# Performance work log

Hardware: AMD Instinct MI355X
Metric: run time of the kernel (lower is better)

The kernel has to match this reference:

```python
import jax, jax.numpy as jnp
import numpy as np

N = 100000          # total nodes
F = 128             # in_features
B = 1000            # number of graphs
NPG = 100           # nodes per graph (contiguous)
DEG = 16            # avg degree
E = B * NPG * DEG   # total edges (intra-graph)
K_RATIO = 0.8
KNUM = max(1, int(K_RATIO * NPG))  # nodes kept per graph = 80


def setup_inputs() -> dict:
    key = jax.random.key(0)
    k1, k2, k3, k4 = jax.random.split(key, 4)
    x = jax.random.normal(k1, (N, F), dtype=jnp.float32)
    # intra-graph random edges: offset each block of NPG*DEG edges by its graph's base node id
    offs = (jnp.arange(E, dtype=jnp.int32) // (NPG * DEG)) * NPG
    src = jax.random.randint(k2, (E,), 0, NPG, dtype=jnp.int32) + offs
    dst = jax.random.randint(k3, (E,), 0, NPG, dtype=jnp.int32) + offs
    edge_index = jnp.stack([src, dst], axis=0)
    batch = (jnp.arange(N, dtype=jnp.int32) // NPG).astype(jnp.int32)
    limit = float(np.sqrt(6.0 / (F + 1)))  # xavier_uniform for (F,1)
    theta_att = jax.random.uniform(k4, (F, 1), dtype=jnp.float32, minval=-limit, maxval=limit)
    return {"x": x, "edge_index": edge_index, "batch": batch, "theta_att": theta_att}


def reference(x, edge_index, batch, theta_att):
    num_nodes = x.shape[0]
    # add self loops with weight 1
    loops = jnp.arange(num_nodes, dtype=edge_index.dtype)
    row = jnp.concatenate([edge_index[0], loops])
    col = jnp.concatenate([edge_index[1], loops])
    w = jnp.ones(row.shape[0], dtype=x.dtype)
    # symmetric degree normalization (degree counted over row, as in torch code)
    deg = jax.ops.segment_sum(w, row, num_segments=num_nodes)
    dis = jnp.where(deg > 0, jax.lax.rsqrt(deg), jnp.zeros((), x.dtype))
    norm = dis[row] * w * dis[col]
    # scatter-add: agg[dst] += x[src] * norm
    agg = jax.ops.segment_sum(x[row] * norm[:, None], col, num_segments=num_nodes)
    z = (agg @ theta_att)[:, 0]                     # (N,)
    # per-graph top-k: graphs are contiguous and equal-sized -> reshape
    zb = z.reshape(B, NPG)
    _, pos = jax.lax.top_k(zb, KNUM)                # (B, KNUM) positions within each graph
    pos = jnp.sort(pos, axis=1)                     # global sort of keep_idx == per-graph sort here
    keep = (pos + jnp.arange(B, dtype=pos.dtype)[:, None] * NPG).reshape(-1)  # (B*KNUM,)
    scale = jax.nn.sigmoid(z[keep])[:, None]
    x_new = x[keep] * scale                         # (B*KNUM, F)
    batch_new = batch[keep]
    # subgraph with relabeled nodes; dropped edges padded with -1 (fixed shape for jit)
    node_mask = jnp.zeros(num_nodes, dtype=bool).at[keep].set(True)
    new_id = jnp.cumsum(node_mask.astype(jnp.int32)) - 1
    emask = node_mask[edge_index[0]] & node_mask[edge_index[1]]
    edge_index_new = jnp.where(emask[None, :], new_id[edge_index], -1)
    return x_new, edge_index_new, batch_new
```

## Files before the change

### kernel.cpp

```cpp
#include <hip/hip_runtime.h>


#define NPG   100
#define EPG   1600
#define KNUM  80
#define FDIM  128
#define BT    512
#define NF4   (NPG * FDIM / 4)
#define NE4   (EPG / 4)
#define NCH   (NF4 / BT)
#define NREM  (NF4 - NCH * BT)
#define P8    9

struct Smem {
    alignas(16) float xB[NPG * FDIM];
    int4   edge4[NE4];
    int    cnt[8][NPG];
    double part[NPG * P8];
    double dis[NPG];
    double a[NPG];
    double zp[8][NPG];
    double z[NPG];
    unsigned long long mask7[8];
    int    newid[NPG];
    float  scalen[NPG];
};

typedef __attribute__((address_space(1))) const unsigned int gu32;
typedef __attribute__((address_space(3))) unsigned int lu32;

__device__ __forceinline__ void bar_nodrain() {
    asm volatile("s_waitcnt lgkmcnt(0)" ::: "memory");
    __builtin_amdgcn_s_barrier();
    asm volatile("" ::: "memory");
}

template<bool FROMLDS, bool PF>
__device__ __forceinline__
void process_graph(Smem& sm, int g, int tid, int wave, int lane, float4 th,
                   float4 (&v)[NCH], float4& vR, int4 es, int4 ed,
                   const float4* pfsrc,
                   float* __restrict__ out, int E_total, int out_x_elems)
{
    const int  base = g * NPG;
    const bool hasE = tid < NE4;
    const bool hasR = tid < NREM;
    int* sh_edge = (int*)sm.edge4;

    {
        int*    cw = sm.cnt[wave];
        double* zw = sm.zp[wave];
        for (int i = lane; i < NPG; i += 64) { cw[i] = 0; zw[i] = 0.0; }
    }

    int4 p;
    if (hasE) {
        int4 s4 = es, d4 = ed;
        s4.x -= base; s4.y -= base; s4.z -= base; s4.w -= base;
        d4.x -= base; d4.y -= base; d4.z -= base; d4.w -= base;
        p.x = s4.x | (d4.x << 16); p.y = s4.y | (d4.y << 16);
        p.z = s4.z | (d4.z << 16); p.w = s4.w | (d4.w << 16);
        sm.edge4[tid] = p;
        int* cw = sm.cnt[wave];
        atomicAdd(&cw[s4.x], 1); atomicAdd(&cw[s4.y], 1);
        atomicAdd(&cw[s4.z], 1); atomicAdd(&cw[s4.w], 1);
    }

    const float4* xl = (const float4*)sm.xB;
    #pragma unroll
    for (int i = 0; i < NCH; ++i) {
        int idx = i * BT + tid;
        if (FROMLDS) v[i] = xl[idx];
        double dp = (double)v[i].x * th.x + (double)v[i].y * th.y
                  + (double)v[i].z * th.z + (double)v[i].w * th.w;
        dp += __shfl_xor(dp, 1, 64);
        dp += __shfl_xor(dp, 2, 64);
        if ((lane & 3) == 0)
            sm.part[(idx >> 5) * P8 + ((idx & 31) >> 2)] = dp;
    }
    if (hasR) {
        int idx = NCH * BT + tid;
        if (FROMLDS) vR = xl[idx];
        double dp = (double)vR.x * th.x + (double)vR.y * th.y
                  + (double)vR.z * th.z + (double)vR.w * th.w;
        dp += __shfl_xor(dp, 1, 64);
        dp += __shfl_xor(dp, 2, 64);
        if ((lane & 3) == 0)
            sm.part[(idx >> 5) * P8 + ((idx & 31) >> 2)] = dp;
    }

    if (PF) {
        #pragma unroll
        for (int i = 0; i < NCH; ++i) {
            int idx = i * BT + tid;
            __builtin_amdgcn_global_load_lds((gu32*)(pfsrc + idx),
                (lu32*)(sm.xB + (size_t)(i * BT + wave * 64) * 4), 16, 0, 0);
        }
        if (wave < 2) {
            int idx = NCH * BT + tid;
            __builtin_amdgcn_global_load_lds((gu32*)(pfsrc + idx),
                (lu32*)(sm.xB + (size_t)(NCH * BT + wave * 64) * 4), 16, 0, 0);
        }
    }
    bar_nodrain();

    if (tid < NPG) {
        const double* pr = sm.part + tid * P8;
        double s = ((pr[0] + pr[1]) + (pr[2] + pr[3]))
                 + ((pr[4] + pr[5]) + (pr[6] + pr[7]));
        int deg = 1 + sm.cnt[0][tid] + sm.cnt[1][tid] + sm.cnt[2][tid]
                    + sm.cnt[3][tid] + sm.cnt[4][tid] + sm.cnt[5][tid]
                    + sm.cnt[6][tid] + sm.cnt[7][tid];
        double dis = 1.0 / sqrt((double)deg);
        sm.dis[tid] = dis;
        sm.a[tid]   = s * dis;
    }
    bar_nodrain();

    {
        double* zw = sm.zp[wave];
        for (int j = tid; j < EPG; j += BT) {
            int e = sh_edge[j];
            atomicAdd(&zw[e >> 16], sm.a[e & 0xffff]);
        }
    }
    bar_nodrain();

    if (tid < NPG) {
        double zi = sm.a[tid]
                  + sm.zp[0][tid] + sm.zp[1][tid] + sm.zp[2][tid] + sm.zp[3][tid]
                  + sm.zp[4][tid] + sm.zp[5][tid] + sm.zp[6][tid] + sm.zp[7][tid];
        sm.z[tid] = zi * sm.dis[tid];
        sm.newid[tid] = -1;
    }
    bar_nodrain();

    const bool rk = tid < 4 * NPG;
    const int  n2 = tid >> 2;
    int r = 0;
    double zn = 0.0;
    if (rk) {
        zn = sm.z[n2];
        const int j0 = (tid & 3) * 25;
        for (int j = j0; j < j0 + 25; ++j) {
            double zj = sm.z[j];
            r += (int)((zj > zn) | ((zj == zn) & (j < n2)));
        }
    }
    r += __shfl_xor(r, 1, 64);
    r += __shfl_xor(r, 2, 64);
    const bool lead = rk && ((tid & 3) == 0) && (r < KNUM);
    unsigned long long m = __ballot(lead);
    if (lane == 0) sm.mask7[wave] = m;
    bar_nodrain();

    if (lead) {
        int before = __popcll(m & ((1ull << lane) - 1ull));
        for (int w2 = 0; w2 < wave; ++w2) before += __popcll(sm.mask7[w2]);
        int row = g * KNUM + before;
        sm.newid[n2]  = row;
        sm.scalen[n2] = 1.0f / (1.0f + __expf(-(float)zn));
        out[(size_t)out_x_elems + 2 * (size_t)E_total + row] = (float)g;
    }
    bar_nodrain();

    float4* outx = (float4*)out;
    #pragma unroll
    for (int i = 0; i < NCH; ++i) {
        int idx = i * BT + tid;
        int nid = sm.newid[idx >> 5];
        if (nid >= 0) {
            float sc = sm.scalen[idx >> 5];
            float4 o;
            o.x = v[i].x * sc; o.y = v[i].y * sc;
            o.z = v[i].z * sc; o.w = v[i].w * sc;
            outx[(size_t)nid * 32 + (idx & 31)] = o;
        }
    }
    if (hasR) {
        int idx = NCH * BT + tid;
        int nid = sm.newid[idx >> 5];
        if (nid >= 0) {
            float sc = sm.scalen[idx >> 5];
            float4 o;
            o.x = vR.x * sc; o.y = vR.y * sc;
            o.z = vR.z * sc; o.w = vR.w * sc;
            outx[(size_t)nid * 32 + (idx & 31)] = o;
        }
    }

    float* e0 = out + out_x_elems;
    float* e1 = e0 + E_total;
    if (hasE) {
        float4 o0, o1;
        {
            int a_ = sm.newid[p.x & 0xffff], b_ = sm.newid[p.x >> 16];
            bool vv = (a_ >= 0) && (b_ >= 0);
            o0.x = vv ? (float)a_ : -1.0f; o1.x = vv ? (float)b_ : -1.0f;
        }
        {
            int a_ = sm.newid[p.y & 0xffff], b_ = sm.newid[p.y >> 16];
            bool vv = (a_ >= 0) && (b_ >= 0);
            o0.y = vv ? (float)a_ : -1.0f; o1.y = vv ? (float)b_ : -1.0f;
        }
        {
            int a_ = sm.newid[p.z & 0xffff], b_ = sm.newid[p.z >> 16];
            bool vv = (a_ >= 0) && (b_ >= 0);
            o0.z = vv ? (float)a_ : -1.0f; o1.z = vv ? (float)b_ : -1.0f;
        }
        {
            int a_ = sm.newid[p.w & 0xffff], b_ = sm.newid[p.w >> 16];
            bool vv = (a_ >= 0) && (b_ >= 0);
            o0.w = vv ? (float)a_ : -1.0f; o1.w = vv ? (float)b_ : -1.0f;
        }
        ((float4*)e0)[(size_t)g * NE4 + tid] = o0;
        ((float4*)e1)[(size_t)g * NE4 + tid] = o1;
    }
}

__global__ __launch_bounds__(BT, 4)
void sagpool_fused8(const float* __restrict__ x,
                    const int*   __restrict__ ei,
                    const float* __restrict__ theta,
                    float* __restrict__ out,
                    int E_total, int out_x_elems, int n_graphs)
{
    __shared__ Smem sm;
    const int tid  = threadIdx.x;
    const int wave = tid >> 6;
    const int lane = tid & 63;
    const int gA   = blockIdx.x * 2;
    const int gB   = gA + 1;
    const bool hasE = tid < NE4;
    const bool hasR = tid < NREM;
    const bool doB  = gB < n_graphs;

    const float4 th = ((const float4*)theta)[lane & 31];

    int4 esA = {0,0,0,0}, edA = {0,0,0,0}, esB = {0,0,0,0}, edB = {0,0,0,0};
    if (hasE) {
        esA = ((const int4*)(ei + (size_t)gA * EPG))[tid];
        edA = ((const int4*)(ei + (size_t)E_total + (size_t)gA * EPG))[tid];
        if (doB) {
            esB = ((const int4*)(ei + (size_t)gB * EPG))[tid];
            edB = ((const int4*)(ei + (size_t)E_total + (size_t)gB * EPG))[tid];
        }
    }
    float4 v[NCH];
    float4 vR = {0.f, 0.f, 0.f, 0.f};
    const float4* xA = (const float4*)(x + (size_t)gA * NPG * FDIM);
    const float4* xB = (const float4*)(x + (size_t)gB * NPG * FDIM);
    #pragma unroll
    for (int i = 0; i < NCH; ++i) v[i] = xA[i * BT + tid];
    if (hasR) vR = xA[NCH * BT + tid];

    process_graph<false, true>(sm, gA, tid, wave, lane, th, v, vR, esA, edA,
                               xB, out, E_total, out_x_elems);
    if (doB) {
        __syncthreads();
        process_graph<true, false>(sm, gB, tid, wave, lane, th, v, vR, esB, edB,
                                   nullptr, out, E_total, out_x_elems);
    }
}

extern "C" void kernel_launch(void* const* d_in, const int* in_sizes, int n_in,
                              void* d_out, int out_size, void* d_ws, size_t ws_size,
                              hipStream_t stream)
{
    const float* x     = (const float*)d_in[0];
    const int*   ei    = (const int*)d_in[1];
    const float* theta = (const float*)d_in[3];
    float* out = (float*)d_out;

    const int N = in_sizes[0] / FDIM;
    const int E = in_sizes[1] / 2;
    const int B = N / NPG;
    const int out_x_elems = B * KNUM * FDIM;
    const int nb = (B + 1) / 2;

    sagpool_fused8<<<dim3(nb), dim3(BT), 0, stream>>>(x, ei, theta, out,
                                                      E, out_x_elems, B);
}
```

Baseline: 112.5 us.

## Overlap graph A output stores with graph B setup and dot-product phase

Restructures the two-graph-per-block kernel so graph A's scaled feature rows and relabeled edges are computed into registers first. Their global stores are then issued after graph B's edge packing and dot products, instead of before graph B starts. The intent is to hide store latency and the full __syncthreads between graphs behind graph B's work, replacing that sync with lighter barriers. In exchange it holds more live registers (nidA plus the edge payloads), which risks spills or lower occupancy under the launch bound of 4.

```diff
diff --git a/kernel.cpp b/kernel.cpp
--- a/kernel.cpp
+++ b/kernel.cpp
@@ -35,74 +35,11 @@
     asm volatile("" ::: "memory");
 }
 
-template<bool FROMLDS, bool PF>
 __device__ __forceinline__
-void process_graph(Smem& sm, int g, int tid, int wave, int lane, float4 th,
-                   float4 (&v)[NCH], float4& vR, int4 es, int4 ed,
-                   const float4* pfsrc,
-                   float* __restrict__ out, int E_total, int out_x_elems)
-{
-    const int  base = g * NPG;
-    const bool hasE = tid < NE4;
-    const bool hasR = tid < NREM;
+void mid_phases(Smem& sm, int g, int tid, int wave, int lane,
+                float* __restrict__ out, int E_total, int out_x_elems)
+{
     int* sh_edge = (int*)sm.edge4;
-
-    {
-        int*    cw = sm.cnt[wave];
-        double* zw = sm.zp[wave];
-        for (int i = lane; i < NPG; i += 64) { cw[i] = 0; zw[i] = 0.0; }
-    }
-
-    int4 p;
-    if (hasE) {
-        int4 s4 = es, d4 = ed;
-        s4.x -= base; s4.y -= base; s4.z -= base; s4.w -= base;
-        d4.x -= base; d4.y -= base; d4.z -= base; d4.w -= base;
-        p.x = s4.x | (d4.x << 16); p.y = s4.y | (d4.y << 16);
-        p.z = s4.z | (d4.z << 16); p.w = s4.w | (d4.w << 16);
-        sm.edge4[tid] = p;
-        int* cw = sm.cnt[wave];
-        atomicAdd(&cw[s4.x], 1); atomicAdd(&cw[s4.y], 1);
-        atomicAdd(&cw[s4.z], 1); atomicAdd(&cw[s4.w], 1);
-    }
-
-    const float4* xl = (const float4*)sm.xB;
-    #pragma unroll
-    for (int i = 0; i < NCH; ++i) {
-        int idx = i * BT + tid;
-        if (FROMLDS) v[i] = xl[idx];
-        double dp = (double)v[i].x * th.x + (double)v[i].y * th.y
-                  + (double)v[i].z * th.z + (double)v[i].w * th.w;
-        dp += __shfl_xor(dp, 1, 64);
-        dp += __shfl_xor(dp, 2, 64);
-        if ((lane & 3) == 0)
-            sm.part[(idx >> 5) * P8 + ((idx & 31) >> 2)] = dp;
-    }
-    if (hasR) {
-        int idx = NCH * BT + tid;
-        if (FROMLDS) vR = xl[idx];
-        double dp = (double)vR.x * th.x + (double)vR.y * th.y
-                  + (double)vR.z * th.z + (double)vR.w * th.w;
-        dp += __shfl_xor(dp, 1, 64);
-        dp += __shfl_xor(dp, 2, 64);
-        if ((lane & 3) == 0)
-            sm.part[(idx >> 5) * P8 + ((idx & 31) >> 2)] = dp;
-    }
-
-    if (PF) {
-        #pragma unroll
-        for (int i = 0; i < NCH; ++i) {
-            int idx = i * BT + tid;
-            __builtin_amdgcn_global_load_lds((gu32*)(pfsrc + idx),
-                (lu32*)(sm.xB + (size_t)(i * BT + wave * 64) * 4), 16, 0, 0);
-        }
-        if (wave < 2) {
-            int idx = NCH * BT + tid;
-            __builtin_amdgcn_global_load_lds((gu32*)(pfsrc + idx),
-                (lu32*)(sm.xB + (size_t)(NCH * BT + wave * 64) * 4), 16, 0, 0);
-        }
-    }
-    bar_nodrain();
 
     if (tid < NPG) {
         const double* pr = sm.part + tid * P8;
@@ -163,63 +100,52 @@
         out[(size_t)out_x_elems + 2 * (size_t)E_total + row] = (float)g;
     }
     bar_nodrain();
-
-    float4* outx = (float4*)out;
-    #pragma unroll
-    for (int i = 0; i < NCH; ++i) {
-        int idx = i * BT + tid;
-        int nid = sm.newid[idx >> 5];
-        if (nid >= 0) {
-            float sc = sm.scalen[idx >> 5];
-            float4 o;
-            o.x = v[i].x * sc; o.y = v[i].y * sc;
-            o.z = v[i].z * sc; o.w = v[i].w * sc;
-            outx[(size_t)nid * 32 + (idx & 31)] = o;
-        }
-    }
-    if (hasR) {
-        int idx = NCH * BT + tid;
-        int nid = sm.newid[idx >> 5];
-        if (nid >= 0) {
-            float sc = sm.scalen[idx >> 5];
-            float4 o;
-            o.x = vR.x * sc; o.y = vR.y * sc;
-            o.z = vR.z * sc; o.w = vR.w * sc;
-            outx[(size_t)nid * 32 + (idx & 31)] = o;
-        }
-    }
-
-    float* e0 = out + out_x_elems;
-    float* e1 = e0 + E_total;
-    if (hasE) {
-        float4 o0, o1;
-        {
-            int a_ = sm.newid[p.x & 0xffff], b_ = sm.newid[p.x >> 16];
-            bool vv = (a_ >= 0) && (b_ >= 0);
-            o0.x = vv ? (float)a_ : -1.0f; o1.x = vv ? (float)b_ : -1.0f;
-        }
-        {
-            int a_ = sm.newid[p.y & 0xffff], b_ = sm.newid[p.y >> 16];
-            bool vv = (a_ >= 0) && (b_ >= 0);
-            o0.y = vv ? (float)a_ : -1.0f; o1.y = vv ? (float)b_ : -1.0f;
-        }
-        {
-            int a_ = sm.newid[p.z & 0xffff], b_ = sm.newid[p.z >> 16];
-            bool vv = (a_ >= 0) && (b_ >= 0);
-            o0.z = vv ? (float)a_ : -1.0f; o1.z = vv ? (float)b_ : -1.0f;
-        }
-        {
-            int a_ = sm.newid[p.w & 0xffff], b_ = sm.newid[p.w >> 16];
-            bool vv = (a_ >= 0) && (b_ >= 0);
-            o0.w = vv ? (float)a_ : -1.0f; o1.w = vv ? (float)b_ : -1.0f;
-        }
-        ((float4*)e0)[(size_t)g * NE4 + tid] = o0;
-        ((float4*)e1)[(size_t)g * NE4 + tid] = o1;
-    }
+}
+
+__device__ __forceinline__
+int4 pack_edges(Smem& sm, int base, int tid, int wave, int4 es, int4 ed)
+{
+    int4 s4 = es, d4 = ed;
+    s4.x -= base; s4.y -= base; s4.z -= base; s4.w -= base;
+    d4.x -= base; d4.y -= base; d4.z -= base; d4.w -= base;
+    int4 p; p.x = s4.x | (d4.x << 16); p.y = s4.y | (d4.y << 16);
+            p.z = s4.z | (d4.z << 16); p.w = s4.w | (d4.w << 16);
+    sm.edge4[tid] = p;
+    int* cw = sm.cnt[wave];
+    atomicAdd(&cw[s4.x], 1); atomicAdd(&cw[s4.y], 1);
+    atomicAdd(&cw[s4.z], 1); atomicAdd(&cw[s4.w], 1);
+    return p;
+}
+
+__device__ __forceinline__
+float4 edge_payload(Smem& sm, int4 p, bool lo)
+{
+    float4 o;
+    {
+        int a_ = sm.newid[p.x & 0xffff], b_ = sm.newid[p.x >> 16];
+        bool vv = (a_ >= 0) && (b_ >= 0);
+        o.x = vv ? (float)(lo ? a_ : b_) : -1.0f;
+    }
+    {
+        int a_ = sm.newid[p.y & 0xffff], b_ = sm.newid[p.y >> 16];
+        bool vv = (a_ >= 0) && (b_ >= 0);
+        o.y = vv ? (float)(lo ? a_ : b_) : -1.0f;
+    }
+    {
+        int a_ = sm.newid[p.z & 0xffff], b_ = sm.newid[p.z >> 16];
+        bool vv = (a_ >= 0) && (b_ >= 0);
+        o.z = vv ? (float)(lo ? a_ : b_) : -1.0f;
+    }
+    {
+        int a_ = sm.newid[p.w & 0xffff], b_ = sm.newid[p.w >> 16];
+        bool vv = (a_ >= 0) && (b_ >= 0);
+        o.w = vv ? (float)(lo ? a_ : b_) : -1.0f;
+    }
+    return o;
 }
 
 __global__ __launch_bounds__(BT, 4)
-void sagpool_fused8(const float* __restrict__ x,
+void sagpool_fused9(const float* __restrict__ x,
                     const int*   __restrict__ ei,
                     const float* __restrict__ theta,
                     float* __restrict__ out,
@@ -236,6 +162,9 @@
     const bool doB  = gB < n_graphs;
 
     const float4 th = ((const float4*)theta)[lane & 31];
+    float4* outx = (float4*)out;
+    float* e0 = out + out_x_elems;
+    float* e1 = e0 + E_total;
 
     int4 esA = {0,0,0,0}, edA = {0,0,0,0}, esB = {0,0,0,0}, edB = {0,0,0,0};
     if (hasE) {
@@ -254,12 +183,172 @@
     for (int i = 0; i < NCH; ++i) v[i] = xA[i * BT + tid];
     if (hasR) vR = xA[NCH * BT + tid];
 
-    process_graph<false, true>(sm, gA, tid, wave, lane, th, v, vR, esA, edA,
-                               xB, out, E_total, out_x_elems);
+    {
+        int*    cw = sm.cnt[wave];
+        double* zw = sm.zp[wave];
+        for (int i = lane; i < NPG; i += 64) { cw[i] = 0; zw[i] = 0.0; }
+    }
+    int4 pA = {0,0,0,0};
+    if (hasE) pA = pack_edges(sm, gA * NPG, tid, wave, esA, edA);
+
+    #pragma unroll
+    for (int i = 0; i < NCH; ++i) {
+        int idx = i * BT + tid;
+        double dp = (double)v[i].x * th.x + (double)v[i].y * th.y
+                  + (double)v[i].z * th.z + (double)v[i].w * th.w;
+        dp += __shfl_xor(dp, 1, 64);
+        dp += __shfl_xor(dp, 2, 64);
+        if ((lane & 3) == 0)
+            sm.part[(idx >> 5) * P8 + ((idx & 31) >> 2)] = dp;
+    }
+    if (hasR) {
+        int idx = NCH * BT + tid;
+        double dp = (double)vR.x * th.x + (double)vR.y * th.y
+                  + (double)vR.z * th.z + (double)vR.w * th.w;
+        dp += __shfl_xor(dp, 1, 64);
+        dp += __shfl_xor(dp, 2, 64);
+        if ((lane & 3) == 0)
+            sm.part[(idx >> 5) * P8 + ((idx & 31) >> 2)] = dp;
+    }
+
     if (doB) {
-        __syncthreads();
-        process_graph<true, false>(sm, gB, tid, wave, lane, th, v, vR, esB, edB,
-                                   nullptr, out, E_total, out_x_elems);
+        #pragma unroll
+        for (int i = 0; i < NCH; ++i) {
+            int idx = i * BT + tid;
+            __builtin_amdgcn_global_load_lds((gu32*)(xB + idx),
+                (lu32*)(sm.xB + (size_t)(i * BT + wave * 64) * 4), 16, 0, 0);
+        }
+        if (wave < 2) {
+            int idx = NCH * BT + tid;
+            __builtin_amdgcn_global_load_lds((gu32*)(xB + idx),
+                (lu32*)(sm.xB + (size_t)(NCH * BT + wave * 64) * 4), 16, 0, 0);
+        }
+    }
+    bar_nodrain();
+
+    mid_phases(sm, gA, tid, wave, lane, out, E_total, out_x_elems);
+
+    int nidA[NCH], nidAR = -1;
+    #pragma unroll
+    for (int i = 0; i < NCH; ++i) {
+        int row = (i * BT + tid) >> 5;
+        int nid = sm.newid[row];
+        nidA[i] = nid;
+        if (nid >= 0) {
+            float sc = sm.scalen[row];
+            v[i].x *= sc; v[i].y *= sc; v[i].z *= sc; v[i].w *= sc;
+        }
+    }
+    if (hasR) {
+        int row = (NCH * BT + tid) >> 5;
+        nidAR = sm.newid[row];
+        if (nidAR >= 0) {
+            float sc = sm.scalen[row];
+            vR.x *= sc; vR.y *= sc; vR.z *= sc; vR.w *= sc;
+        }
+    }
+    float4 o0A = {0,0,0,0}, o1A = {0,0,0,0};
+    if (hasE) {
+        o0A = edge_payload(sm, pA, true);
+        o1A = edge_payload(sm, pA, false);
+    }
+    bar_nodrain();
+
+    if (!doB) {
+        #pragma unroll
+        for (int i = 0; i < NCH; ++i) {
+            int idx = i * BT + tid;
+            if (nidA[i] >= 0) outx[(size_t)nidA[i] * 32 + (idx & 31)] = v[i];
+        }
+        if (hasR && nidAR >= 0)
+            outx[(size_t)nidAR * 32 + ((NCH * BT + tid) & 31)] = vR;
+        if (hasE) {
+            ((float4*)e0)[(size_t)gA * NE4 + tid] = o0A;
+            ((float4*)e1)[(size_t)gA * NE4 + tid] = o1A;
+        }
+        return;
+    }
+
+    {
+        int*    cw = sm.cnt[wave];
+        double* zw = sm.zp[wave];
+        for (int i = lane; i < NPG; i += 64) { cw[i] = 0; zw[i] = 0.0; }
+    }
+    int4 pB = {0,0,0,0};
+    if (hasE) pB = pack_edges(sm, gB * NPG, tid, wave, esB, edB);
+
+    asm volatile("s_waitcnt vmcnt(0)" ::: "memory");
+
+    const float4* xl = (const float4*)sm.xB;
+    #pragma unroll
+    for (int i = 0; i < NCH; ++i) {
+        int idx = i * BT + tid;
+        float4 w4 = xl[idx];
+        double dp = (double)w4.x * th.x + (double)w4.y * th.y
+                  + (double)w4.z * th.z + (double)w4.w * th.w;
+        dp += __shfl_xor(dp, 1, 64);
+        dp += __shfl_xor(dp, 2, 64);
+        if ((lane & 3) == 0)
+            sm.part[(idx >> 5) * P8 + ((idx & 31) >> 2)] = dp;
+    }
+    if (hasR) {
+        int idx = NCH * BT + tid;
+        float4 w4 = xl[idx];
+        double dp = (double)w4.x * th.x + (double)w4.y * th.y
+                  + (double)w4.z * th.z + (double)w4.w * th.w;
+        dp += __shfl_xor(dp, 1, 64);
+        dp += __shfl_xor(dp, 2, 64);
+        if ((lane & 3) == 0)
+            sm.part[(idx >> 5) * P8 + ((idx & 31) >> 2)] = dp;
+    }
+
+    #pragma unroll
+    for (int i = 0; i < NCH; ++i) {
+        int idx = i * BT + tid;
+        if (nidA[i] >= 0) outx[(size_t)nidA[i] * 32 + (idx & 31)] = v[i];
+    }
+    if (hasR && nidAR >= 0)
+        outx[(size_t)nidAR * 32 + ((NCH * BT + tid) & 31)] = vR;
+    if (hasE) {
+        ((float4*)e0)[(size_t)gA * NE4 + tid] = o0A;
+        ((float4*)e1)[(size_t)gA * NE4 + tid] = o1A;
+    }
+    bar_nodrain();
+
+    mid_phases(sm, gB, tid, wave, lane, out, E_total, out_x_elems);
+
+    #pragma unroll
+    for (int i = 0; i < NCH; ++i) {
+        int idx = i * BT + tid;
+        int row = idx >> 5;
+        int nid = sm.newid[row];
+        if (nid >= 0) {
+            float sc = sm.scalen[row];
+            float4 w4 = xl[idx];
+            float4 o;
+            o.x = w4.x * sc; o.y = w4.y * sc;
+            o.z = w4.z * sc; o.w = w4.w * sc;
+            outx[(size_t)nid * 32 + (idx & 31)] = o;
+        }
+    }
+    if (hasR) {
+        int idx = NCH * BT + tid;
+        int row = idx >> 5;
+        int nid = sm.newid[row];
+        if (nid >= 0) {
+            float sc = sm.scalen[row];
+            float4 w4 = xl[idx];
+            float4 o;
+            o.x = w4.x * sc; o.y = w4.y * sc;
+            o.z = w4.z * sc; o.w = w4.w * sc;
+            outx[(size_t)nid * 32 + (idx & 31)] = o;
+        }
+    }
+    if (hasE) {
+        float4 o0B = edge_payload(sm, pB, true);
+        float4 o1B = edge_payload(sm, pB, false);
+        ((float4*)e0)[(size_t)gB * NE4 + tid] = o0B;
+        ((float4*)e1)[(size_t)gB * NE4 + tid] = o1B;
     }
 }
 
@@ -278,6 +367,6 @@
     const int out_x_elems = B * KNUM * FDIM;
     const int nb = (B + 1) / 2;
 
-    sagpool_fused8<<<dim3(nb), dim3(BT), 0, stream>>>(x, ei, theta, out,
+    sagpool_fused9<<<dim3(nb), dim3(BT), 0, stream>>>(x, ei, theta, out,
                                                       E, out_x_elems, B);
 }
```

New measurement: 113.2 us. Within noise of the previous version (+0.6%).

## Replace LDS top-k bookkeeping with per-wave redundant ranking and bpermute lookups

Applied to the files above, without the earlier changes.

Each wave now computes all 100 node scores redundantly and ranks them itself, covering two nodes per lane, and keeps the new ids and sigmoid scales in registers. Edge and row remapping then reads them with ds_bpermute instead of LDS tables. This removes two block barriers and the cross-wave mask exchange. Other changes: the dot-product partials are reduced over 8 lanes instead of 4, the z partial buffers are double-buffered per graph so the inter-graph __syncthreads can go, and the second graph's edge loads are deferred into the prefetch phase. In exchange every wave does the full O(N^2) ranking, and the second graph's x rows are re-read from LDS.

```diff
diff --git a/kernel.cpp b/kernel.cpp
--- a/kernel.cpp
+++ b/kernel.cpp
@@ -10,20 +10,17 @@
 #define NE4   (EPG / 4)
 #define NCH   (NF4 / BT)
 #define NREM  (NF4 - NCH * BT)
-#define P8    9
+#define P4    5
 
 struct Smem {
     alignas(16) float xB[NPG * FDIM];
     int4   edge4[NE4];
     int    cnt[8][NPG];
-    double part[NPG * P8];
+    double part[NPG * P4];
+    double zs[8][NPG];
     double dis[NPG];
     double a[NPG];
-    double zp[8][NPG];
-    double z[NPG];
-    unsigned long long mask7[8];
-    int    newid[NPG];
-    float  scalen[NPG];
+    double zp[2][4][NPG];
 };
 
 typedef __attribute__((address_space(1))) const unsigned int gu32;
@@ -35,25 +32,62 @@
     asm volatile("" ::: "memory");
 }
 
+__device__ __forceinline__ int bperm_i(int idx, int lo, int hi) {
+    int l = __builtin_amdgcn_ds_bpermute((idx & 63) << 2, lo);
+    int h = __builtin_amdgcn_ds_bpermute((idx & 63) << 2, hi);
+    return idx < 64 ? l : h;
+}
+__device__ __forceinline__ float bperm_f(int idx, float lo, float hi) {
+    int l = __builtin_amdgcn_ds_bpermute((idx & 63) << 2, __float_as_int(lo));
+    int h = __builtin_amdgcn_ds_bpermute((idx & 63) << 2, __float_as_int(hi));
+    return __int_as_float(idx < 64 ? l : h);
+}
+
 template<bool FROMLDS, bool PF>
 __device__ __forceinline__
-void process_graph(Smem& sm, int g, int tid, int wave, int lane, float4 th,
-                   float4 (&v)[NCH], float4& vR, int4 es, int4 ed,
-                   const float4* pfsrc,
+void process_graph(Smem& sm, int g, int gp, int tid, int wave, int lane,
+                   float4 th, float4 (&v)[NCH], float4& vR, int4 es, int4 ed,
+                   const float4* pfsrc, const int* ei, int4& esB, int4& edB,
                    float* __restrict__ out, int E_total, int out_x_elems)
 {
     const int  base = g * NPG;
     const bool hasE = tid < NE4;
     const bool hasR = tid < NREM;
     int* sh_edge = (int*)sm.edge4;
+    const float4* xl = (const float4*)sm.xB;
 
     {
         int*    cw = sm.cnt[wave];
-        double* zw = sm.zp[wave];
-        for (int i = lane; i < NPG; i += 64) { cw[i] = 0; zw[i] = 0.0; }
-    }
-
-    int4 p;
+        double* zw = sm.zp[gp][wave >> 1];
+        for (int i = lane; i < NPG; i += 64) cw[i] = 0;
+        for (int i = lane; i < NPG; i += 64) zw[i] = 0.0;
+    }
+
+    #pragma unroll
+    for (int i = 0; i < NCH; ++i) {
+        int idx = i * BT + tid;
+        if (FROMLDS) v[i] = xl[idx];
+        double dp = (double)v[i].x * th.x + (double)v[i].y * th.y
+                  + (double)v[i].z * th.z + (double)v[i].w * th.w;
+        dp += __shfl_xor(dp, 1, 64);
+        dp += __shfl_xor(dp, 2, 64);
+        dp += __shfl_xor(dp, 4, 64);
+        if ((lane & 7) == 0)
+            sm.part[(idx >> 5) * P4 + ((lane & 31) >> 3)] = dp;
+    }
+    if (hasR) {
+        int idx = NCH * BT + tid;
+        if (FROMLDS) vR = xl[idx];
+        double dp = (double)vR.x * th.x + (double)vR.y * th.y
+                  + (double)vR.z * th.z + (double)vR.w * th.w;
+        dp += __shfl_xor(dp, 1, 64);
+        dp += __shfl_xor(dp, 2, 64);
+        dp += __shfl_xor(dp, 4, 64);
+        if ((lane & 7) == 0)
+            sm.part[(idx >> 5) * P4 + ((lane & 31) >> 3)] = dp;
+    }
+
+    int4 p = {0, 0, 0, 0};
     if (hasE) {
         int4 s4 = es, d4 = ed;
         s4.x -= base; s4.y -= base; s4.z -= base; s4.w -= base;
@@ -66,29 +100,6 @@
         atomicAdd(&cw[s4.z], 1); atomicAdd(&cw[s4.w], 1);
     }
 
-    const float4* xl = (const float4*)sm.xB;
-    #pragma unroll
-    for (int i = 0; i < NCH; ++i) {
-        int idx = i * BT + tid;
-        if (FROMLDS) v[i] = xl[idx];
-        double dp = (double)v[i].x * th.x + (double)v[i].y * th.y
-                  + (double)v[i].z * th.z + (double)v[i].w * th.w;
-        dp += __shfl_xor(dp, 1, 64);
-        dp += __shfl_xor(dp, 2, 64);
-        if ((lane & 3) == 0)
-            sm.part[(idx >> 5) * P8 + ((idx & 31) >> 2)] = dp;
-    }
-    if (hasR) {
-        int idx = NCH * BT + tid;
-        if (FROMLDS) vR = xl[idx];
-        double dp = (double)vR.x * th.x + (double)vR.y * th.y
-                  + (double)vR.z * th.z + (double)vR.w * th.w;
-        dp += __shfl_xor(dp, 1, 64);
-        dp += __shfl_xor(dp, 2, 64);
-        if ((lane & 3) == 0)
-            sm.part[(idx >> 5) * P8 + ((idx & 31) >> 2)] = dp;
-    }
-
     if (PF) {
         #pragma unroll
         for (int i = 0; i < NCH; ++i) {
@@ -101,13 +112,16 @@
             __builtin_amdgcn_global_load_lds((gu32*)(pfsrc + idx),
                 (lu32*)(sm.xB + (size_t)(NCH * BT + wave * 64) * 4), 16, 0, 0);
         }
+        if (hasE) {
+            esB = ((const int4*)(ei + (size_t)(g + 1) * EPG))[tid];
+            edB = ((const int4*)(ei + (size_t)E_total + (size_t)(g + 1) * EPG))[tid];
+        }
     }
     bar_nodrain();
 
     if (tid < NPG) {
-        const double* pr = sm.part + tid * P8;
-        double s = ((pr[0] + pr[1]) + (pr[2] + pr[3]))
-                 + ((pr[4] + pr[5]) + (pr[6] + pr[7]));
+        const double* pr = sm.part + tid * P4;
+        double s = (pr[0] + pr[1]) + (pr[2] + pr[3]);
         int deg = 1 + sm.cnt[0][tid] + sm.cnt[1][tid] + sm.cnt[2][tid]
                     + sm.cnt[3][tid] + sm.cnt[4][tid] + sm.cnt[5][tid]
                     + sm.cnt[6][tid] + sm.cnt[7][tid];
@@ -118,7 +132,7 @@
     bar_nodrain();
 
     {
-        double* zw = sm.zp[wave];
+        double* zw = sm.zp[gp][wave >> 1];
         for (int j = tid; j < EPG; j += BT) {
             int e = sh_edge[j];
             atomicAdd(&zw[e >> 16], sm.a[e & 0xffff]);
@@ -126,104 +140,117 @@
     }
     bar_nodrain();
 
-    if (tid < NPG) {
-        double zi = sm.a[tid]
-                  + sm.zp[0][tid] + sm.zp[1][tid] + sm.zp[2][tid] + sm.zp[3][tid]
-                  + sm.zp[4][tid] + sm.zp[5][tid] + sm.zp[6][tid] + sm.zp[7][tid];
-        sm.z[tid] = zi * sm.dis[tid];
-        sm.newid[tid] = -1;
-    }
-    bar_nodrain();
-
-    const bool rk = tid < 4 * NPG;
-    const int  n2 = tid >> 2;
-    int r = 0;
-    double zn = 0.0;
-    if (rk) {
-        zn = sm.z[n2];
-        const int j0 = (tid & 3) * 25;
-        for (int j = j0; j < j0 + 25; ++j) {
-            double zj = sm.z[j];
-            r += (int)((zj > zn) | ((zj == zn) & (j < n2)));
-        }
-    }
-    r += __shfl_xor(r, 1, 64);
-    r += __shfl_xor(r, 2, 64);
-    const bool lead = rk && ((tid & 3) == 0) && (r < KNUM);
-    unsigned long long m = __ballot(lead);
-    if (lane == 0) sm.mask7[wave] = m;
-    bar_nodrain();
-
-    if (lead) {
-        int before = __popcll(m & ((1ull << lane) - 1ull));
-        for (int w2 = 0; w2 < wave; ++w2) before += __popcll(sm.mask7[w2]);
-        int row = g * KNUM + before;
-        sm.newid[n2]  = row;
-        sm.scalen[n2] = 1.0f / (1.0f + __expf(-(float)zn));
-        out[(size_t)out_x_elems + 2 * (size_t)E_total + row] = (float)g;
-    }
-    bar_nodrain();
+    const double* zq0 = sm.zp[gp][0];
+    const double* zq1 = sm.zp[gp][1];
+    const double* zq2 = sm.zp[gp][2];
+    const double* zq3 = sm.zp[gp][3];
+    double zlo = (sm.a[lane] + zq0[lane] + zq1[lane] + zq2[lane] + zq3[lane])
+               * sm.dis[lane];
+    const bool hiv = lane < (NPG - 64);
+    const int  nh  = 64 + lane;
+    double zhi = -1.0e300;
+    if (hiv)
+        zhi = (sm.a[nh] + zq0[nh] + zq1[nh] + zq2[nh] + zq3[nh]) * sm.dis[nh];
+    double* zw = sm.zs[wave];
+    zw[lane] = zlo;
+    if (hiv) zw[nh] = zhi;
+
+    int rlo = 0, rhi = 0;
+    #pragma unroll 4
+    for (int j = 0; j < NPG; ++j) {
+        double zj = zw[j];
+        rlo += (int)((zj > zlo) | ((zj == zlo) & (j < lane)));
+        rhi += (int)((zj > zhi) | ((zj == zhi) & (j < nh)));
+    }
+    const bool klo = rlo < KNUM;
+    const bool khi = hiv && (rhi < KNUM);
+    unsigned long long mlo = __ballot(klo);
+    unsigned long long mhi = __ballot(khi);
+    unsigned long long below = (1ull << lane) - 1ull;
+    int nlo = klo ? g * KNUM + __popcll(mlo & below) : -1;
+    int nhi = khi ? g * KNUM + __popcll(mlo) + __popcll(mhi & below) : -1;
+    float slo = 1.0f / (1.0f + __expf(-(float)zlo));
+    float shi = 1.0f / (1.0f + __expf(-(float)zhi));
+
+    if (PF)
+        asm volatile("s_waitcnt vmcnt(0)" ::: "memory");
+
+    if (wave == 0) {
+        float* bn = out + (size_t)out_x_elems + 2 * (size_t)E_total;
+        if (klo) bn[nlo] = (float)g;
+        if (khi) bn[nhi] = (float)g;
+    }
 
     float4* outx = (float4*)out;
     #pragma unroll
     for (int i = 0; i < NCH; ++i) {
         int idx = i * BT + tid;
-        int nid = sm.newid[idx >> 5];
+        int row = idx >> 5;
+        int nid = bperm_i(row, nlo, nhi);
+        float sc = bperm_f(row, slo, shi);
         if (nid >= 0) {
-            float sc = sm.scalen[idx >> 5];
+            float4 w4 = FROMLDS ? xl[idx] : v[i];
             float4 o;
-            o.x = v[i].x * sc; o.y = v[i].y * sc;
-            o.z = v[i].z * sc; o.w = v[i].w * sc;
+            o.x = w4.x * sc; o.y = w4.y * sc;
+            o.z = w4.z * sc; o.w = w4.w * sc;
             outx[(size_t)nid * 32 + (idx & 31)] = o;
         }
     }
     if (hasR) {
         int idx = NCH * BT + tid;
-        int nid = sm.newid[idx >> 5];
+        int row = idx >> 5;
+        int nid = bperm_i(row, nlo, nhi);
+        float sc = bperm_f(row, slo, shi);
         if (nid >= 0) {
-            float sc = sm.scalen[idx >> 5];
+            float4 w4 = FROMLDS ? xl[idx] : vR;
             float4 o;
-            o.x = vR.x * sc; o.y = vR.y * sc;
-            o.z = vR.z * sc; o.w = vR.w * sc;
+            o.x = w4.x * sc; o.y = w4.y * sc;
+            o.z = w4.z * sc; o.w = w4.w * sc;
             outx[(size_t)nid * 32 + (idx & 31)] = o;
         }
     }
 
-    float* e0 = out + out_x_elems;
-    float* e1 = e0 + E_total;
-    if (hasE) {
+    {
         float4 o0, o1;
         {
-            int a_ = sm.newid[p.x & 0xffff], b_ = sm.newid[p.x >> 16];
-            bool vv = (a_ >= 0) && (b_ >= 0);
-            o0.x = vv ? (float)a_ : -1.0f; o1.x = vv ? (float)b_ : -1.0f;
+            int na = bperm_i(p.x & 0xffff, nlo, nhi);
+            int nb = bperm_i(p.x >> 16,    nlo, nhi);
+            bool vv = (na >= 0) && (nb >= 0);
+            o0.x = vv ? (float)na : -1.0f; o1.x = vv ? (float)nb : -1.0f;
         }
         {
-            int a_ = sm.newid[p.y & 0xffff], b_ = sm.newid[p.y >> 16];
-            bool vv = (a_ >= 0) && (b_ >= 0);
-            o0.y = vv ? (float)a_ : -1.0f; o1.y = vv ? (float)b_ : -1.0f;
+            int na = bperm_i(p.y & 0xffff, nlo, nhi);
+            int nb = bperm_i(p.y >> 16,    nlo, nhi);
+            bool vv = (na >= 0) && (nb >= 0);
+            o0.y = vv ? (float)na : -1.0f; o1.y = vv ? (float)nb : -1.0f;
         }
         {
-            int a_ = sm.newid[p.z & 0xffff], b_ = sm.newid[p.z >> 16];
-            bool vv = (a_ >= 0) && (b_ >= 0);
-            o0.z = vv ? (float)a_ : -1.0f; o1.z = vv ? (float)b_ : -1.0f;
+            int na = bperm_i(p.z & 0xffff, nlo, nhi);
+            int nb = bperm_i(p.z >> 16,    nlo, nhi);
+            bool vv = (na >= 0) && (nb >= 0);
+            o0.z = vv ? (float)na : -1.0f; o1.z = vv ? (float)nb : -1.0f;
         }
         {
-            int a_ = sm.newid[p.w & 0xffff], b_ = sm.newid[p.w >> 16];
-            bool vv = (a_ >= 0) && (b_ >= 0);
-            o0.w = vv ? (float)a_ : -1.0f; o1.w = vv ? (float)b_ : -1.0f;
-        }
-        ((float4*)e0)[(size_t)g * NE4 + tid] = o0;
-        ((float4*)e1)[(size_t)g * NE4 + tid] = o1;
+            int na = bperm_i(p.w & 0xffff, nlo, nhi);
+            int nb = bperm_i(p.w >> 16,    nlo, nhi);
+            bool vv = (na >= 0) && (nb >= 0);
+            o0.w = vv ? (float)na : -1.0f; o1.w = vv ? (float)nb : -1.0f;
+        }
+        if (hasE) {
+            float* e0 = out + out_x_elems;
+            float* e1 = e0 + E_total;
+            ((float4*)e0)[(size_t)g * NE4 + tid] = o0;
+            ((float4*)e1)[(size_t)g * NE4 + tid] = o1;
+        }
     }
 }
 
 __global__ __launch_bounds__(BT, 4)
-void sagpool_fused8(const float* __restrict__ x,
-                    const int*   __restrict__ ei,
-                    const float* __restrict__ theta,
-                    float* __restrict__ out,
-                    int E_total, int out_x_elems, int n_graphs)
+void sagpool_fused10(const float* __restrict__ x,
+                     const int*   __restrict__ ei,
+                     const float* __restrict__ theta,
+                     float* __restrict__ out,
+                     int E_total, int out_x_elems, int n_graphs)
 {
     __shared__ Smem sm;
     const int tid  = threadIdx.x;
@@ -237,30 +264,27 @@
 
     const float4 th = ((const float4*)theta)[lane & 31];
 
+    float4 v[NCH];
+    float4 vR = {0.f, 0.f, 0.f, 0.f};
+    const float4* xA = (const float4*)(x + (size_t)gA * NPG * FDIM);
+    #pragma unroll
+    for (int i = 0; i < NCH; ++i) v[i] = xA[i * BT + tid];
+    if (hasR) vR = xA[NCH * BT + tid];
+
     int4 esA = {0,0,0,0}, edA = {0,0,0,0}, esB = {0,0,0,0}, edB = {0,0,0,0};
     if (hasE) {
         esA = ((const int4*)(ei + (size_t)gA * EPG))[tid];
         edA = ((const int4*)(ei + (size_t)E_total + (size_t)gA * EPG))[tid];
-        if (doB) {
-            esB = ((const int4*)(ei + (size_t)gB * EPG))[tid];
-            edB = ((const int4*)(ei + (size_t)E_total + (size_t)gB * EPG))[tid];
-        }
-    }
-    float4 v[NCH];
-    float4 vR = {0.f, 0.f, 0.f, 0.f};
-    const float4* xA = (const float4*)(x + (size_t)gA * NPG * FDIM);
+    }
+
     const float4* xB = (const float4*)(x + (size_t)gB * NPG * FDIM);
-    #pragma unroll
-    for (int i = 0; i < NCH; ++i) v[i] = xA[i * BT + tid];
-    if (hasR) vR = xA[NCH * BT + tid];
-
-    process_graph<false, true>(sm, gA, tid, wave, lane, th, v, vR, esA, edA,
-                               xB, out, E_total, out_x_elems);
-    if (doB) {
-        __syncthreads();
-        process_graph<true, false>(sm, gB, tid, wave, lane, th, v, vR, esB, edB,
-                                   nullptr, out, E_total, out_x_elems);
-    }
+    process_graph<false, true>(sm, gA, 0, tid, wave, lane, th, v, vR,
+                               esA, edA, xB, ei, esB, edB,
+                               out, E_total, out_x_elems);
+    if (doB)
+        process_graph<true, false>(sm, gB, 1, tid, wave, lane, th, v, vR,
+                                   esB, edB, nullptr, ei, esB, edB,
+                                   out, E_total, out_x_elems);
 }
 
 extern "C" void kernel_launch(void* const* d_in, const int* in_sizes, int n_in,
@@ -278,6 +302,6 @@
     const int out_x_elems = B * KNUM * FDIM;
     const int nb = (B + 1) / 2;
 
-    sagpool_fused8<<<dim3(nb), dim3(BT), 0, stream>>>(x, ei, theta, out,
-                                                      E, out_x_elems, B);
-}
+    sagpool_fused10<<<dim3(nb), dim3(BT), 0, stream>>>(x, ei, theta, out,
+                                                       E, out_x_elems, B);
+}
```

New measurement: 123.7 us. 10.0% more time.
